# Optimization experiments

Measured on AMD Instinct MI355X. Metric: run time of the kernel, lower is better.

The kernel has to match this reference:

```python
import jax, jax.numpy as jnp
from jax import lax
import numpy as np

V, E, H, B, L = 50000, 100, 512, 1024, 128


def _gru_params(key, E, H, dtype=jnp.float32):
    k = 1.0 / np.sqrt(H)
    ks = jax.random.split(key, 4)
    Wih = jax.random.uniform(ks[0], (3 * H, E), dtype, -k, k)
    Whh = jax.random.uniform(ks[1], (3 * H, H), dtype, -k, k)
    bih = jax.random.uniform(ks[2], (3 * H,), dtype, -k, k)
    bhh = jax.random.uniform(ks[3], (3 * H,), dtype, -k, k)
    return Wih, Whh, bih, bhh


def setup_inputs() -> dict:
    key = jax.random.key(0)
    kc, kr, kec, ker, kgc, kgr = jax.random.split(key, 6)
    contexts = jax.random.randint(kc, (B, L), 0, V)
    replies = jax.random.randint(kr, (B, L), 0, V)
    ctx_emb = jax.random.uniform(kec, (V, E), jnp.float32, -0.25, 0.25)
    rep_emb = jax.random.uniform(ker, (V, E), jnp.float32, -0.25, 0.25)
    ctx_Wih, ctx_Whh, ctx_bih, ctx_bhh = _gru_params(kgc, E, H)
    rep_Wih, rep_Whh, rep_bih, rep_bhh = _gru_params(kgr, E, H)
    return dict(contexts=contexts, replies=replies,
                ctx_emb=ctx_emb, ctx_Wih=ctx_Wih, ctx_Whh=ctx_Whh, ctx_bih=ctx_bih, ctx_bhh=ctx_bhh,
                rep_emb=rep_emb, rep_Wih=rep_Wih, rep_Whh=rep_Whh, rep_bih=rep_bih, rep_bhh=rep_bhh)


def _gru_backward_last(x, Wih, Whh, bih, bhh):
    """Final hidden of the backward direction of a bidirectional GRU.
    x: [B, L, E] -> h: [B, H]. enc_h_t[-1] in torch == reverse-direction final state,
    i.e. a GRU run over the time-reversed sequence."""
    Bsz = x.shape[0]
    Hh = Whh.shape[1]
    xs = jnp.swapaxes(x, 0, 1)[::-1]  # [L, B, E], reversed time

    def step(h, xt):
        gi = xt @ Wih.T + bih          # [B, 3H]
        gh = h @ Whh.T + bhh           # [B, 3H]
        i_r, i_z, i_n = jnp.split(gi, 3, axis=-1)
        h_r, h_z, h_n = jnp.split(gh, 3, axis=-1)
        r = jax.nn.sigmoid(i_r + h_r)
        z = jax.nn.sigmoid(i_z + h_z)
        n = jnp.tanh(i_n + r * h_n)
        h_new = (1.0 - z) * n + z * h
        return h_new, None

    h0 = jnp.zeros((Bsz, Hh), x.dtype)
    h_last, _ = lax.scan(step, h0, xs)
    return h_last


def reference(contexts, replies,
              ctx_emb, ctx_Wih, ctx_Whh, ctx_bih, ctx_bhh,
              rep_emb, rep_Wih, rep_Whh, rep_bih, rep_bhh):
    # embedding lookup (dropout is identity at eval)
    ex_c = ctx_emb[contexts]  # [B, L, E]
    ex_r = rep_emb[replies]   # [B, L, E]
    hc = _gru_backward_last(ex_c, ctx_Wih, ctx_Whh, ctx_bih, ctx_bhh)  # [B, H]
    hr = _gru_backward_last(ex_r, rep_Wih, rep_Whh, rep_bih, rep_bhh)  # [B, H]
    # fused equivalent of the nested-loop per-pair dot products + row softmax
    scores = hc @ hr.T  # [B, B]
    return jax.nn.softmax(scores, axis=-1)
```

## Files before the change

### kernel.cpp

```cpp
#include <hip/hip_runtime.h>
#include <math.h>

#define B_SZ   1024
#define H_SZ   512
#define E_SZ   100
#define L_SZ   128
#define KX     128
#define VOCAB  50000

typedef _Float16 f16x8 __attribute__((ext_vector_type(8)));
typedef float    f32x4 __attribute__((ext_vector_type(4)));

#define MFMA16(a, b, c) __builtin_amdgcn_mfma_f32_16x16x32_f16((a), (b), (c), 0, 0, 0)

__device__ __forceinline__ float fast_sigmoid(float x) {
    return __builtin_amdgcn_rcpf(1.0f + __expf(-x));
}
__device__ __forceinline__ float fast_tanh(float x) {
    return 1.0f - 2.0f * __builtin_amdgcn_rcpf(1.0f + __expf(2.0f * x));
}

__global__ __launch_bounds__(256) void prep_emb_kernel(
    _Float16* __restrict__ ef_c, const float* __restrict__ e_c,
    _Float16* __restrict__ ef_r, const float* __restrict__ e_r)
{
    const int PER = VOCAB * KX;
    int idx = blockIdx.x * 256 + threadIdx.x;
    if (idx >= 2 * PER) return;
    const int gru = idx >= PER;
    const int local = gru ? idx - PER : idx;
    const int v = local >> 7;
    const int e = local & 127;
    const float* src = gru ? e_r : e_c;
    _Float16* dst = gru ? ef_r : ef_c;
    dst[local] = (_Float16)(e < E_SZ ? src[v * E_SZ + e] : 0.0f);
}

struct GruArgs {
    const float* Whh[2];
    const float* Wih[2];
    const float* bih[2];
    const float* bhh[2];
    const _Float16* emb[2];
    const int* idx[2];
    _Float16* hA;
    _Float16* hB;
    unsigned int* bars;
    unsigned int* claim;
};

__global__ __launch_bounds__(512, 2) void gru_persistent(GruArgs args)
{
    __shared__ int role_s;
    if (threadIdx.x == 0) {
        unsigned xcd;
        asm volatile("s_getreg_b32 %0, hwreg(HW_REG_XCC_ID)" : "=s"(xcd));
        xcd &= 7u;
        unsigned slot = atomicAdd(&args.claim[xcd], 1u);
        role_s = (int)(xcd * 32u + slot);
    }
    __syncthreads();
    const int role = role_s;
    const int grp  = role >> 4;
    const int ut   = role & 15;
    const int gru  = grp >> 3;
    const int mt   = grp & 7;

    const float* __restrict__ Whh = args.Whh[gru];
    const float* __restrict__ Wih = args.Wih[gru];
    const float* __restrict__ bih = args.bih[gru];
    const float* __restrict__ bhh = args.bhh[gru];
    const _Float16* __restrict__ embf = args.emb[gru];
    const int* __restrict__ idx = args.idx[gru];

    const int u0 = ut * 32;
    const int mB = mt * 128;

    __shared__ _Float16 Wl[7680 * 8];

    for (int f = threadIdx.x; f < 7680; f += 512) {
        const int ln  = f & 63;
        const int q   = f >> 6;
        const int kc  = q / 6;
        const int rem = q - kc * 6;
        const int g   = rem >> 1;
        const int u2  = rem & 1;
        const int row = g * H_SZ + u0 + u2 * 16 + (ln & 15);
        const int ks  = ln >> 4;
        _Float16 tmp[8];
        if (kc < 16) {
            const float* src = Whh + (size_t)row * H_SZ + kc * 32 + ks * 8;
#pragma unroll
            for (int j = 0; j < 8; ++j) tmp[j] = (_Float16)src[j];
        } else {
            const int e = (kc - 16) * 32 + ks * 8;
#pragma unroll
            for (int j = 0; j < 8; ++j)
                tmp[j] = (_Float16)((e + j < E_SZ) ? Wih[(size_t)row * E_SZ + e + j]
                                                   : 0.0f);
        }
        *(f16x8*)&Wl[(size_t)f * 8] = *(const f16x8*)tmp;
    }
    __syncthreads();

    const int lane = threadIdx.x & 63;
    const int wave = threadIdx.x >> 6;
    const int lr   = lane & 15;
    const int kseg = lane >> 4;
    const int mw   = mB + wave * 16;

    const _Float16* Wbase = Wl + (size_t)lane * 8;
#define WFRAG(kc, g, u2) \
    (*(const f16x8*)(Wbase + (size_t)((((kc) * 3 + (g)) * 2 + (u2)) * 64) * 8))

    float bir[2], biz[2], binn[2], bhn[2];
    int ucol[2];
#pragma unroll
    for (int u2 = 0; u2 < 2; ++u2) {
        ucol[u2] = u0 + u2 * 16 + lr;
        const int u = ucol[u2];
        bir[u2]  = bih[u]             + bhh[u];
        biz[u2]  = bih[H_SZ + u]      + bhh[H_SZ + u];
        binn[u2] = bih[2 * H_SZ + u];
        bhn[u2]  = bhh[2 * H_SZ + u];
    }

    _Float16* hbuf0 = args.hA + (size_t)gru * B_SZ * H_SZ;
    _Float16* hbuf1 = args.hB + (size_t)gru * B_SZ * H_SZ;
    unsigned int* bar = args.bars + grp * 32;

    float hreg[2][4] = {};

#pragma unroll 1
    for (int step = 0; step < L_SZ; ++step) {
        const _Float16* __restrict__ hin = (step & 1) ? hbuf1 : hbuf0;
        _Float16* __restrict__ hout      = (step & 1) ? hbuf0 : hbuf1;
        const int lcol = L_SZ - 1 - step;

        f32x4 accr[2], accz[2], acchn[2], accin[2];
#pragma unroll
        for (int j = 0; j < 2; j++) {
            accr[j]  = (f32x4){0.f, 0.f, 0.f, 0.f};
            accz[j]  = (f32x4){0.f, 0.f, 0.f, 0.f};
            acchn[j] = (f32x4){0.f, 0.f, 0.f, 0.f};
            accin[j] = (f32x4){0.f, 0.f, 0.f, 0.f};
        }

        const int iv0 = idx[(mw + lr) * L_SZ + lcol];
#pragma unroll
        for (int xc = 0; xc < 4; ++xc) {
            const int e0 = xc * 32 + kseg * 8;
            f16x8 a0 = *(const f16x8*)(embf + (size_t)iv0 * KX + e0);
#pragma unroll
            for (int u2 = 0; u2 < 2; ++u2) {
                f16x8 b0 = WFRAG(16 + xc, 0, u2);
                f16x8 b1 = WFRAG(16 + xc, 1, u2);
                f16x8 b2 = WFRAG(16 + xc, 2, u2);
                accr[u2]  = MFMA16(a0, b0, accr[u2]);
                accz[u2]  = MFMA16(a0, b1, accz[u2]);
                accin[u2] = MFMA16(a0, b2, accin[u2]);
            }
        }

        if (step > 0) {
            if (threadIdx.x == 0) {
                const unsigned tgt = 16u * (unsigned)step;
                while (__hip_atomic_load(bar, __ATOMIC_RELAXED,
                                         __HIP_MEMORY_SCOPE_AGENT) < tgt)
                    __builtin_amdgcn_s_sleep(1);
            }
            __syncthreads();
        }

        const _Float16* hrow0 = hin + (mw + lr) * H_SZ + kseg * 8;
        f16x8 a0h[16];
        asm volatile(
            "global_load_dwordx4 %0,  %16, off sc0\n\t"
            "global_load_dwordx4 %1,  %16, off offset:64 sc0\n\t"
            "global_load_dwordx4 %2,  %16, off offset:128 sc0\n\t"
            "global_load_dwordx4 %3,  %16, off offset:192 sc0\n\t"
            "global_load_dwordx4 %4,  %16, off offset:256 sc0\n\t"
            "global_load_dwordx4 %5,  %16, off offset:320 sc0\n\t"
            "global_load_dwordx4 %6,  %16, off offset:384 sc0\n\t"
            "global_load_dwordx4 %7,  %16, off offset:448 sc0\n\t"
            "global_load_dwordx4 %8,  %16, off offset:512 sc0\n\t"
            "global_load_dwordx4 %9,  %16, off offset:576 sc0\n\t"
            "global_load_dwordx4 %10, %16, off offset:640 sc0\n\t"
            "global_load_dwordx4 %11, %16, off offset:704 sc0\n\t"
            "global_load_dwordx4 %12, %16, off offset:768 sc0\n\t"
            "global_load_dwordx4 %13, %16, off offset:832 sc0\n\t"
            "global_load_dwordx4 %14, %16, off offset:896 sc0\n\t"
            "global_load_dwordx4 %15, %16, off offset:960 sc0\n\t"
            "s_waitcnt vmcnt(0)"
            : "=&v"(a0h[0]),  "=&v"(a0h[1]),  "=&v"(a0h[2]),  "=&v"(a0h[3]),
              "=&v"(a0h[4]),  "=&v"(a0h[5]),  "=&v"(a0h[6]),  "=&v"(a0h[7]),
              "=&v"(a0h[8]),  "=&v"(a0h[9]),  "=&v"(a0h[10]), "=&v"(a0h[11]),
              "=&v"(a0h[12]), "=&v"(a0h[13]), "=&v"(a0h[14]), "=&v"(a0h[15])
            : "v"(hrow0)
            : "memory");

#pragma unroll
        for (int kc = 0; kc < 16; ++kc) {
#pragma unroll
            for (int u2 = 0; u2 < 2; ++u2) {
                f16x8 b0 = WFRAG(kc, 0, u2);
                f16x8 b1 = WFRAG(kc, 1, u2);
                f16x8 b2 = WFRAG(kc, 2, u2);
                accr[u2]  = MFMA16(a0h[kc], b0, accr[u2]);
                accz[u2]  = MFMA16(a0h[kc], b1, accz[u2]);
                acchn[u2] = MFMA16(a0h[kc], b2, acchn[u2]);
            }
        }

#pragma unroll
        for (int u2 = 0; u2 < 2; ++u2) {
#pragma unroll
            for (int r = 0; r < 4; ++r) {
                const int m = mw + kseg * 4 + r;
                const float rg = fast_sigmoid(accr[u2][r] + bir[u2]);
                const float zg = fast_sigmoid(accz[u2][r] + biz[u2]);
                const float ng = fast_tanh(accin[u2][r] + binn[u2] +
                                           rg * (acchn[u2][r] + bhn[u2]));
                float nh = (1.0f - zg) * ng + zg * hreg[u2][r];
                nh = (float)(_Float16)nh;
                hreg[u2][r] = nh;
                hout[m * H_SZ + ucol[u2]] = (_Float16)nh;
            }
        }

        if (step + 1 < L_SZ) {
            __syncthreads();
            if (threadIdx.x == 0) {
                __hip_atomic_fetch_add(bar, 1u, __ATOMIC_RELAXED,
                                       __HIP_MEMORY_SCOPE_AGENT);
            }
        }
    }
#undef WFRAG
}

__global__ __launch_bounds__(256, 1) void scores_kernel(
    const _Float16* __restrict__ hc, const _Float16* __restrict__ hr,
    float* __restrict__ out)
{
    const int lane = threadIdx.x & 63;
    const int wave = threadIdx.x >> 6;
    const int lr   = lane & 15;
    const int kseg = lane >> 4;
    const int m0 = blockIdx.y * 64 + (wave >> 1) * 32;
    const int n0 = blockIdx.x * 64 + (wave & 1) * 32;

    f32x4 acc[2][2];
#pragma unroll
    for (int i = 0; i < 2; i++)
#pragma unroll
        for (int j = 0; j < 2; j++)
            acc[i][j] = (f32x4){0.f, 0.f, 0.f, 0.f};

#pragma unroll 2
    for (int kc = 0; kc < 16; kc++) {
        const int k0 = kc * 32 + kseg * 8;
        f16x8 a[2], b[2];
#pragma unroll
        for (int mt = 0; mt < 2; mt++)
            a[mt] = *(const f16x8*)(hc + (m0 + mt * 16 + lr) * H_SZ + k0);
#pragma unroll
        for (int nt = 0; nt < 2; nt++)
            b[nt] = *(const f16x8*)(hr + (n0 + nt * 16 + lr) * H_SZ + k0);
#pragma unroll
        for (int mt = 0; mt < 2; mt++)
#pragma unroll
            for (int nt = 0; nt < 2; nt++)
                acc[mt][nt] = MFMA16(a[mt], b[nt], acc[mt][nt]);
    }

#pragma unroll
    for (int mt = 0; mt < 2; mt++)
#pragma unroll
        for (int nt = 0; nt < 2; nt++)
#pragma unroll
            for (int r = 0; r < 4; r++) {
                const int m = m0 + mt * 16 + kseg * 4 + r;
                const int n = n0 + nt * 16 + lr;
                out[m * B_SZ + n] = acc[mt][nt][r];
            }
}

__global__ __launch_bounds__(256) void softmax_kernel(float* __restrict__ out)
{
    const int row = blockIdx.x;
    float* p = out + (size_t)row * B_SZ;
    const int t = threadIdx.x;
    const int wave = t >> 6;
    const int lane = t & 63;

    float4 v = ((const float4*)p)[t];
    float m = fmaxf(fmaxf(v.x, v.y), fmaxf(v.z, v.w));
#pragma unroll
    for (int off = 32; off >= 1; off >>= 1)
        m = fmaxf(m, __shfl_xor(m, off, 64));

    __shared__ float redm[4];
    if (lane == 0) redm[wave] = m;
    __syncthreads();
    m = fmaxf(fmaxf(redm[0], redm[1]), fmaxf(redm[2], redm[3]));

    const float e0 = __expf(v.x - m);
    const float e1 = __expf(v.y - m);
    const float e2 = __expf(v.z - m);
    const float e3 = __expf(v.w - m);
    float s = e0 + e1 + e2 + e3;
#pragma unroll
    for (int off = 32; off >= 1; off >>= 1)
        s += __shfl_xor(s, off, 64);

    __shared__ float reds[4];
    if (lane == 0) reds[wave] = s;
    __syncthreads();
    s = reds[0] + reds[1] + reds[2] + reds[3];

    const float inv = 1.0f / s;
    float4 o;
    o.x = e0 * inv; o.y = e1 * inv; o.z = e2 * inv; o.w = e3 * inv;
    ((float4*)p)[t] = o;
}

extern "C" void kernel_launch(void* const* d_in, const int* in_sizes, int n_in,
                              void* d_out, int out_size, void* d_ws, size_t ws_size,
                              hipStream_t stream)
{
    (void)in_sizes; (void)n_in; (void)out_size; (void)ws_size;

    const int*   contexts = (const int*)d_in[0];
    const int*   replies  = (const int*)d_in[1];
    const float* ctx_emb  = (const float*)d_in[2];
    const float* ctx_Wih  = (const float*)d_in[3];
    const float* ctx_Whh  = (const float*)d_in[4];
    const float* ctx_bih  = (const float*)d_in[5];
    const float* ctx_bhh  = (const float*)d_in[6];
    const float* rep_emb  = (const float*)d_in[7];
    const float* rep_Wih  = (const float*)d_in[8];
    const float* rep_Whh  = (const float*)d_in[9];
    const float* rep_bih  = (const float*)d_in[10];
    const float* rep_bhh  = (const float*)d_in[11];
    float* out = (float*)d_out;

    const size_t EMB_ELEMS = (size_t)VOCAB * KX;
    const size_t H_ELEMS   = (size_t)B_SZ * H_SZ;

    _Float16* base   = (_Float16*)d_ws;
    _Float16* embf_c = base;
    _Float16* embf_r = embf_c + EMB_ELEMS;
    _Float16* hB     = embf_r + EMB_ELEMS;
    _Float16* hA     = hB + 2 * H_ELEMS;
    unsigned int* bars  = (unsigned int*)(hA + 2 * H_ELEMS);
    unsigned int* claim = bars + 16 * 32;

    hipMemsetAsync(hA, 0,
                   2 * H_ELEMS * sizeof(_Float16) +
                   (16 * 32 + 8) * sizeof(unsigned int), stream);

    {
        const int total_emb = 2 * (int)EMB_ELEMS;
        prep_emb_kernel<<<(total_emb + 255) / 256, 256, 0, stream>>>(
            embf_c, ctx_emb, embf_r, rep_emb);
    }

    GruArgs a;
    a.Whh[0] = ctx_Whh; a.Whh[1] = rep_Whh;
    a.Wih[0] = ctx_Wih; a.Wih[1] = rep_Wih;
    a.bih[0] = ctx_bih; a.bih[1] = rep_bih;
    a.bhh[0] = ctx_bhh; a.bhh[1] = rep_bhh;
    a.emb[0] = embf_c;  a.emb[1] = embf_r;
    a.idx[0] = contexts; a.idx[1] = replies;
    a.hA = hA; a.hB = hB; a.bars = bars; a.claim = claim;
    gru_persistent<<<dim3(256), dim3(512), 0, stream>>>(a);

    scores_kernel<<<dim3(B_SZ / 64, B_SZ / 64), 256, 0, stream>>>(hA, hA + H_ELEMS, out);
    softmax_kernel<<<B_SZ, 256, 0, stream>>>(out);
}
```

Before: 1.056 ms.

## Remap waves to 32 rows by 16 units and prefetch next-step embeddings

```diff
diff --git a/kernel.cpp b/kernel.cpp
--- a/kernel.cpp
+++ b/kernel.cpp
@@ -107,35 +107,45 @@
     const int wave = threadIdx.x >> 6;
     const int lr   = lane & 15;
     const int kseg = lane >> 4;
-    const int mw   = mB + wave * 16;
+    const int ms   = wave >> 1;
+    const int u2w  = wave & 1;
+    const int mw   = mB + ms * 32;
 
     const _Float16* Wbase = Wl + (size_t)lane * 8;
 #define WFRAG(kc, g, u2) \
     (*(const f16x8*)(Wbase + (size_t)((((kc) * 3 + (g)) * 2 + (u2)) * 64) * 8))
 
-    float bir[2], biz[2], binn[2], bhn[2];
-    int ucol[2];
-#pragma unroll
-    for (int u2 = 0; u2 < 2; ++u2) {
-        ucol[u2] = u0 + u2 * 16 + lr;
-        const int u = ucol[u2];
-        bir[u2]  = bih[u]             + bhh[u];
-        biz[u2]  = bih[H_SZ + u]      + bhh[H_SZ + u];
-        binn[u2] = bih[2 * H_SZ + u];
-        bhn[u2]  = bhh[2 * H_SZ + u];
-    }
+    const int ucol = u0 + u2w * 16 + lr;
+    const float bir  = bih[ucol]            + bhh[ucol];
+    const float biz  = bih[H_SZ + ucol]     + bhh[H_SZ + ucol];
+    const float binn = bih[2 * H_SZ + ucol];
+    const float bhn  = bhh[2 * H_SZ + ucol];
 
     _Float16* hbuf0 = args.hA + (size_t)gru * B_SZ * H_SZ;
     _Float16* hbuf1 = args.hB + (size_t)gru * B_SZ * H_SZ;
     unsigned int* bar = args.bars + grp * 32;
 
     float hreg[2][4] = {};
+
+    f16x8 er0, er1, er2, er3, es0, es1, es2, es3;
+    int ivn0, ivn1;
+    {
+        const int iv_a = idx[(mw + lr) * L_SZ + (L_SZ - 1)];
+        const int iv_b = idx[(mw + 16 + lr) * L_SZ + (L_SZ - 1)];
+        const _Float16* ea = embf + (size_t)iv_a * KX + kseg * 8;
+        const _Float16* eb = embf + (size_t)iv_b * KX + kseg * 8;
+        er0 = *(const f16x8*)(ea);      er1 = *(const f16x8*)(ea + 32);
+        er2 = *(const f16x8*)(ea + 64); er3 = *(const f16x8*)(ea + 96);
+        es0 = *(const f16x8*)(eb);      es1 = *(const f16x8*)(eb + 32);
+        es2 = *(const f16x8*)(eb + 64); es3 = *(const f16x8*)(eb + 96);
+        ivn0 = idx[(mw + lr) * L_SZ + (L_SZ - 2)];
+        ivn1 = idx[(mw + 16 + lr) * L_SZ + (L_SZ - 2)];
+    }
 
 #pragma unroll 1
     for (int step = 0; step < L_SZ; ++step) {
         const _Float16* __restrict__ hin = (step & 1) ? hbuf1 : hbuf0;
         _Float16* __restrict__ hout      = (step & 1) ? hbuf0 : hbuf1;
-        const int lcol = L_SZ - 1 - step;
 
         f32x4 accr[2], accz[2], acchn[2], accin[2];
 #pragma unroll
@@ -146,20 +156,21 @@
             accin[j] = (f32x4){0.f, 0.f, 0.f, 0.f};
         }
 
-        const int iv0 = idx[(mw + lr) * L_SZ + lcol];
 #pragma unroll
         for (int xc = 0; xc < 4; ++xc) {
-            const int e0 = xc * 32 + kseg * 8;
-            f16x8 a0 = *(const f16x8*)(embf + (size_t)iv0 * KX + e0);
-#pragma unroll
-            for (int u2 = 0; u2 < 2; ++u2) {
-                f16x8 b0 = WFRAG(16 + xc, 0, u2);
-                f16x8 b1 = WFRAG(16 + xc, 1, u2);
-                f16x8 b2 = WFRAG(16 + xc, 2, u2);
-                accr[u2]  = MFMA16(a0, b0, accr[u2]);
-                accz[u2]  = MFMA16(a0, b1, accz[u2]);
-                accin[u2] = MFMA16(a0, b2, accin[u2]);
-            }
+            const f16x8 ea = (xc == 0) ? er0 : (xc == 1) ? er1
+                           : (xc == 2) ? er2 : er3;
+            const f16x8 eb = (xc == 0) ? es0 : (xc == 1) ? es1
+                           : (xc == 2) ? es2 : es3;
+            f16x8 b0 = WFRAG(16 + xc, 0, u2w);
+            f16x8 b1 = WFRAG(16 + xc, 1, u2w);
+            f16x8 b2 = WFRAG(16 + xc, 2, u2w);
+            accr[0]  = MFMA16(ea, b0, accr[0]);
+            accr[1]  = MFMA16(eb, b0, accr[1]);
+            accz[0]  = MFMA16(ea, b1, accz[0]);
+            accz[1]  = MFMA16(eb, b1, accz[1]);
+            accin[0] = MFMA16(ea, b2, accin[0]);
+            accin[1] = MFMA16(eb, b2, accin[1]);
         }
 
         if (step > 0) {
@@ -173,58 +184,92 @@
         }
 
         const _Float16* hrow0 = hin + (mw + lr) * H_SZ + kseg * 8;
-        f16x8 a0h[16];
+        const _Float16* hrow1 = hin + (mw + 16 + lr) * H_SZ + kseg * 8;
+        f16x8 a0h[16], a1h[16];
         asm volatile(
-            "global_load_dwordx4 %0,  %16, off sc0\n\t"
-            "global_load_dwordx4 %1,  %16, off offset:64 sc0\n\t"
-            "global_load_dwordx4 %2,  %16, off offset:128 sc0\n\t"
-            "global_load_dwordx4 %3,  %16, off offset:192 sc0\n\t"
-            "global_load_dwordx4 %4,  %16, off offset:256 sc0\n\t"
-            "global_load_dwordx4 %5,  %16, off offset:320 sc0\n\t"
-            "global_load_dwordx4 %6,  %16, off offset:384 sc0\n\t"
-            "global_load_dwordx4 %7,  %16, off offset:448 sc0\n\t"
-            "global_load_dwordx4 %8,  %16, off offset:512 sc0\n\t"
-            "global_load_dwordx4 %9,  %16, off offset:576 sc0\n\t"
-            "global_load_dwordx4 %10, %16, off offset:640 sc0\n\t"
-            "global_load_dwordx4 %11, %16, off offset:704 sc0\n\t"
-            "global_load_dwordx4 %12, %16, off offset:768 sc0\n\t"
-            "global_load_dwordx4 %13, %16, off offset:832 sc0\n\t"
-            "global_load_dwordx4 %14, %16, off offset:896 sc0\n\t"
-            "global_load_dwordx4 %15, %16, off offset:960 sc0\n\t"
+            "global_load_dwordx4 %0,  %32, off sc0\n\t"
+            "global_load_dwordx4 %1,  %32, off offset:64 sc0\n\t"
+            "global_load_dwordx4 %2,  %32, off offset:128 sc0\n\t"
+            "global_load_dwordx4 %3,  %32, off offset:192 sc0\n\t"
+            "global_load_dwordx4 %4,  %32, off offset:256 sc0\n\t"
+            "global_load_dwordx4 %5,  %32, off offset:320 sc0\n\t"
+            "global_load_dwordx4 %6,  %32, off offset:384 sc0\n\t"
+            "global_load_dwordx4 %7,  %32, off offset:448 sc0\n\t"
+            "global_load_dwordx4 %8,  %32, off offset:512 sc0\n\t"
+            "global_load_dwordx4 %9,  %32, off offset:576 sc0\n\t"
+            "global_load_dwordx4 %10, %32, off offset:640 sc0\n\t"
+            "global_load_dwordx4 %11, %32, off offset:704 sc0\n\t"
+            "global_load_dwordx4 %12, %32, off offset:768 sc0\n\t"
+            "global_load_dwordx4 %13, %32, off offset:832 sc0\n\t"
+            "global_load_dwordx4 %14, %32, off offset:896 sc0\n\t"
+            "global_load_dwordx4 %15, %32, off offset:960 sc0\n\t"
+            "global_load_dwordx4 %16, %33, off sc0\n\t"
+            "global_load_dwordx4 %17, %33, off offset:64 sc0\n\t"
+            "global_load_dwordx4 %18, %33, off offset:128 sc0\n\t"
+            "global_load_dwordx4 %19, %33, off offset:192 sc0\n\t"
+            "global_load_dwordx4 %20, %33, off offset:256 sc0\n\t"
+            "global_load_dwordx4 %21, %33, off offset:320 sc0\n\t"
+            "global_load_dwordx4 %22, %33, off offset:384 sc0\n\t"
+            "global_load_dwordx4 %23, %33, off offset:448 sc0\n\t"
+            "global_load_dwordx4 %24, %33, off offset:512 sc0\n\t"
+            "global_load_dwordx4 %25, %33, off offset:576 sc0\n\t"
+            "global_load_dwordx4 %26, %33, off offset:640 sc0\n\t"
+            "global_load_dwordx4 %27, %33, off offset:704 sc0\n\t"
+            "global_load_dwordx4 %28, %33, off offset:768 sc0\n\t"
+            "global_load_dwordx4 %29, %33, off offset:832 sc0\n\t"
+            "global_load_dwordx4 %30, %33, off offset:896 sc0\n\t"
+            "global_load_dwordx4 %31, %33, off offset:960 sc0\n\t"
             "s_waitcnt vmcnt(0)"
             : "=&v"(a0h[0]),  "=&v"(a0h[1]),  "=&v"(a0h[2]),  "=&v"(a0h[3]),
               "=&v"(a0h[4]),  "=&v"(a0h[5]),  "=&v"(a0h[6]),  "=&v"(a0h[7]),
               "=&v"(a0h[8]),  "=&v"(a0h[9]),  "=&v"(a0h[10]), "=&v"(a0h[11]),
-              "=&v"(a0h[12]), "=&v"(a0h[13]), "=&v"(a0h[14]), "=&v"(a0h[15])
-            : "v"(hrow0)
+              "=&v"(a0h[12]), "=&v"(a0h[13]), "=&v"(a0h[14]), "=&v"(a0h[15]),
+              "=&v"(a1h[0]),  "=&v"(a1h[1]),  "=&v"(a1h[2]),  "=&v"(a1h[3]),
+              "=&v"(a1h[4]),  "=&v"(a1h[5]),  "=&v"(a1h[6]),  "=&v"(a1h[7]),
+              "=&v"(a1h[8]),  "=&v"(a1h[9]),  "=&v"(a1h[10]), "=&v"(a1h[11]),
+              "=&v"(a1h[12]), "=&v"(a1h[13]), "=&v"(a1h[14]), "=&v"(a1h[15])
+            : "v"(hrow0), "v"(hrow1)
             : "memory");
 
+        {
+            const _Float16* ea = embf + (size_t)ivn0 * KX + kseg * 8;
+            const _Float16* eb = embf + (size_t)ivn1 * KX + kseg * 8;
+            er0 = *(const f16x8*)(ea);      er1 = *(const f16x8*)(ea + 32);
+            er2 = *(const f16x8*)(ea + 64); er3 = *(const f16x8*)(ea + 96);
+            es0 = *(const f16x8*)(eb);      es1 = *(const f16x8*)(eb + 32);
+            es2 = *(const f16x8*)(eb + 64); es3 = *(const f16x8*)(eb + 96);
+            int lc = L_SZ - 3 - step;
+            if (lc < 0) lc = 0;
+            ivn0 = idx[(mw + lr) * L_SZ + lc];
+            ivn1 = idx[(mw + 16 + lr) * L_SZ + lc];
+        }
+
 #pragma unroll
         for (int kc = 0; kc < 16; ++kc) {
-#pragma unroll
-            for (int u2 = 0; u2 < 2; ++u2) {
-                f16x8 b0 = WFRAG(kc, 0, u2);
-                f16x8 b1 = WFRAG(kc, 1, u2);
-                f16x8 b2 = WFRAG(kc, 2, u2);
-                accr[u2]  = MFMA16(a0h[kc], b0, accr[u2]);
-                accz[u2]  = MFMA16(a0h[kc], b1, accz[u2]);
-                acchn[u2] = MFMA16(a0h[kc], b2, acchn[u2]);
-            }
-        }
-
-#pragma unroll
-        for (int u2 = 0; u2 < 2; ++u2) {
+            f16x8 b0 = WFRAG(kc, 0, u2w);
+            f16x8 b1 = WFRAG(kc, 1, u2w);
+            f16x8 b2 = WFRAG(kc, 2, u2w);
+            accr[0]  = MFMA16(a0h[kc], b0, accr[0]);
+            accr[1]  = MFMA16(a1h[kc], b0, accr[1]);
+            accz[0]  = MFMA16(a0h[kc], b1, accz[0]);
+            accz[1]  = MFMA16(a1h[kc], b1, accz[1]);
+            acchn[0] = MFMA16(a0h[kc], b2, acchn[0]);
+            acchn[1] = MFMA16(a1h[kc], b2, acchn[1]);
+        }
+
+#pragma unroll
+        for (int m2 = 0; m2 < 2; ++m2) {
 #pragma unroll
             for (int r = 0; r < 4; ++r) {
-                const int m = mw + kseg * 4 + r;
-                const float rg = fast_sigmoid(accr[u2][r] + bir[u2]);
-                const float zg = fast_sigmoid(accz[u2][r] + biz[u2]);
-                const float ng = fast_tanh(accin[u2][r] + binn[u2] +
-                                           rg * (acchn[u2][r] + bhn[u2]));
-                float nh = (1.0f - zg) * ng + zg * hreg[u2][r];
+                const int m = mw + m2 * 16 + kseg * 4 + r;
+                const float rg = fast_sigmoid(accr[m2][r] + bir);
+                const float zg = fast_sigmoid(accz[m2][r] + biz);
+                const float ng = fast_tanh(accin[m2][r] + binn +
+                                           rg * (acchn[m2][r] + bhn));
+                float nh = (1.0f - zg) * ng + zg * hreg[m2][r];
                 nh = (float)(_Float16)nh;
-                hreg[u2][r] = nh;
-                hout[m * H_SZ + ucol[u2]] = (_Float16)nh;
+                hreg[m2][r] = nh;
+                hout[m * H_SZ + ucol] = (_Float16)nh;
             }
         }
 
```

After: 1.465 ms. +38.7%, slower.
